# Performance work log

Hardware: AMD Instinct MI355X
Metric: run time of the kernel (lower is better)

Reference implementation:

```python
import jax, jax.numpy as jnp
import numpy as np

TAU = 100.0
DT = 1.0
NOISE_STD = 0.1
HID = 100


def setup_inputs() -> dict:
    key = jax.random.key(0)
    ks = jax.random.split(key, 7)
    T, B = 750, 1024
    input_seq = jax.random.normal(ks[0], (T, B, 4), dtype=jnp.float32)
    noise = jax.random.normal(ks[1], (T, B, HID), dtype=jnp.float32)
    # orthogonal recurrent weight J [H, H]
    a = jax.random.normal(ks[2], (HID, HID), dtype=jnp.float32)
    q, r = jnp.linalg.qr(a)
    J_w = q * jnp.sign(jnp.diag(r))[None, :]
    # input projection rows [b_m; b_c; b_cm; b_cc] -> [4, H] (xavier for (H,1) fan)
    bound_b = float(np.sqrt(6.0 / (HID + 1)))
    Bmat = jax.random.uniform(ks[3], (4, HID), jnp.float32, -bound_b, bound_b)
    c_x = jnp.zeros((HID,), dtype=jnp.float32)
    bound_w = float(np.sqrt(6.0 / (HID + 1)))
    Wout_w = jax.random.uniform(ks[4], (1, HID), jnp.float32, -bound_w, bound_w)
    Wout_b = jnp.zeros((1,), dtype=jnp.float32)
    return {"input_seq": input_seq, "noise": noise, "J_w": J_w,
            "Bmat": Bmat, "c_x": c_x, "Wout_w": Wout_w, "Wout_b": Wout_b}


def reference(input_seq, noise, J_w, Bmat, c_x, Wout_w, Wout_b):
    # input_seq: [T, B, 4], noise: [T, B, H]
    T, B, _ = input_seq.shape
    alpha = DT / TAU

    # precompute input drive for all steps: u_m@b_m^T + ... == u_t @ Bmat  [T, B, H]
    drive = jnp.einsum('tbi,ih->tbh', input_seq, Bmat)

    def step(x, inp):
        d_t, n_t = inp
        r = jnp.tanh(x)
        dx = alpha * (-x + r @ J_w.T + d_t + c_x + NOISE_STD * n_t)
        x = x + dx
        return x, None

    x0 = jnp.zeros((B, HID), dtype=input_seq.dtype)
    x_final, _ = jax.lax.scan(step, x0, (drive, noise))
    out = jnp.tanh(x_final) @ Wout_w.T + Wout_b  # [B, 1]
    return out.squeeze(-1)  # [B]
```

## Files before the change

kernel.cpp:

```cpp
#include <hip/hip_runtime.h>
#include <hip/hip_bf16.h>

#define HID 100
#define TT 750
#define NB_TOT 1024
#define ALPHA 0.01f
#define NSTD 0.1f

typedef __bf16 bf16x8 __attribute__((ext_vector_type(8)));
typedef float floatx4 __attribute__((ext_vector_type(4)));

__device__ __forceinline__ float fast_tanh(float v) {
    float e = __expf(2.0f * v);
    return 1.0f - 2.0f / (e + 1.0f);
}

__device__ __forceinline__ void wg_barrier() {
    asm volatile("s_waitcnt lgkmcnt(0)" ::: "memory");
    __builtin_amdgcn_s_barrier();
    asm volatile("" ::: "memory");
    __builtin_amdgcn_sched_barrier(0);
}

__global__ __launch_bounds__(256, 2)
void rnn_kernel(const float* __restrict__ useq,
                const float* __restrict__ noise,
                const float* __restrict__ Jw,
                const float* __restrict__ Bm,
                const float* __restrict__ cxp,
                const float* __restrict__ Ww,
                const float* __restrict__ Wb,
                float* __restrict__ out)
{
    __shared__ __align__(16) __bf16 rbuf[16 * 128];
    __shared__ float ybuf[2][112];
    __shared__ float red[256];

    const int tid  = threadIdx.x;
    const int wv   = tid >> 6;
    const int lane = tid & 63;
    const int wg   = blockIdx.x;

    const int  bb  = tid / 100;
    const int  hh  = tid % 100;
    const bool upd = (tid < 200);
    const int  gb  = wg * 2 + bb;

    float bm0=0.f, bm1=0.f, bm2=0.f, bm3=0.f, cx=0.f, wout=0.f;
    if (upd) {
        bm0 = Bm[0*HID + hh]; bm1 = Bm[1*HID + hh];
        bm2 = Bm[2*HID + hh]; bm3 = Bm[3*HID + hh];
        cx  = cxp[hh];
        wout = Ww[hh];
    }

    {
        floatx4 z = {0.f, 0.f, 0.f, 0.f};
        ((floatx4*)rbuf)[tid] = z;
    }

    const int m16 = lane & 15;
    const int q   = lane >> 4;
    bf16x8 jhi[2][4], jlo[2][4];
    #pragma unroll
    for (int ti = 0; ti < 2; ++ti) {
        const int tile = wv * 2 + ti;
        const int h = tile * 16 + m16;
        #pragma unroll
        for (int s = 0; s < 4; ++s) {
            bf16x8 vhi, vlo;
            #pragma unroll
            for (int j = 0; j < 8; ++j) {
                const int k = s * 32 + q * 8 + j;
                float v = (h < HID && k < HID) ? Jw[h * HID + k] : 0.0f;
                __bf16 hi = (__bf16)v;
                vhi[j] = hi;
                vlo[j] = (__bf16)(v - (float)hi);
            }
            jhi[ti][s] = vhi;
            jlo[ti][s] = vlo;
        }
    }

    const float* np = noise + (size_t)gb * HID + hh;
    const float* up = useq  + (size_t)gb * 4;
    float   nb0=0.f, nb1=0.f, nb2=0.f, nb3=0.f;
    floatx4 ub0={0,0,0,0}, ub1={0,0,0,0}, ub2={0,0,0,0}, ub3={0,0,0,0};
    if (upd) {
        nb0 = np[0 * (NB_TOT*HID)]; ub0 = *(const floatx4*)(up + 0 * (NB_TOT*4));
        nb1 = np[1 * (NB_TOT*HID)]; ub1 = *(const floatx4*)(up + 1 * (NB_TOT*4));
        nb2 = np[2 * (NB_TOT*HID)]; ub2 = *(const floatx4*)(up + 2 * (NB_TOT*4));
        nb3 = np[3 * (NB_TOT*HID)]; ub3 = *(const floatx4*)(up + 3 * (NB_TOT*4));
    }

    float x = 0.0f;
    __syncthreads();

    auto step = [&](int T, float& NB, floatx4& UB) {
        bf16x8 afr[4];
        const bf16x8* rb16 = (const bf16x8*)rbuf;
        #pragma unroll
        for (int s = 0; s < 4; ++s)
            afr[s] = rb16[m16 * 16 + ((s * 4 + q) ^ (lane & 7))];
        #pragma unroll
        for (int ti = 0; ti < 2; ++ti) {
            floatx4 acch = {0.f, 0.f, 0.f, 0.f};
            floatx4 accl = {0.f, 0.f, 0.f, 0.f};
            #pragma unroll
            for (int s = 0; s < 4; ++s) {
                acch = __builtin_amdgcn_mfma_f32_16x16x32_bf16(afr[s], jhi[ti][s], acch, 0, 0, 0);
                accl = __builtin_amdgcn_mfma_f32_16x16x32_bf16(afr[s], jlo[ti][s], accl, 0, 0, 0);
            }
            const int tile = wv * 2 + ti;
            if (tile < 7 && lane < 16) {
                ybuf[0][tile * 16 + lane] = acch[0] + accl[0];
                ybuf[1][tile * 16 + lane] = acch[1] + accl[1];
            }
        }
        wg_barrier();
        if (upd) {
            const float y = ybuf[bb][hh];
            const float d = UB[0]*bm0 + UB[1]*bm1 + UB[2]*bm2 + UB[3]*bm3;
            x = x * (1.0f - ALPHA) + ALPHA * (y + d + cx + NSTD * NB);
            const float r = fast_tanh(x);
            rbuf[bb * 128 + (((hh >> 3) ^ bb) << 3) + (hh & 7)] = (__bf16)r;
            const int tf = (T + 4 < TT) ? (T + 4) : (TT - 1);
            NB = np[tf * (NB_TOT*HID)];
            UB = *(const floatx4*)(up + tf * (NB_TOT*4));
        }
        wg_barrier();
    };

    for (int tb = 0; tb < 748; tb += 4) {
        step(tb + 0, nb0, ub0);
        step(tb + 1, nb1, ub1);
        step(tb + 2, nb2, ub2);
        step(tb + 3, nb3, ub3);
    }
    step(748, nb0, ub0);
    step(749, nb1, ub1);

    red[tid] = upd ? (fast_tanh(x) * wout) : 0.0f;
    __syncthreads();
    if (tid < 2) {
        float s2 = Wb[0];
        #pragma unroll 4
        for (int i = 0; i < HID; ++i) s2 += red[tid * HID + i];
        out[wg * 2 + tid] = s2;
    }
}

extern "C" void kernel_launch(void* const* d_in, const int* in_sizes, int n_in,
                              void* d_out, int out_size, void* d_ws, size_t ws_size,
                              hipStream_t stream) {
    rnn_kernel<<<dim3(512), dim3(256), 0, stream>>>(
        (const float*)d_in[0], (const float*)d_in[1], (const float*)d_in[2],
        (const float*)d_in[3], (const float*)d_in[4], (const float*)d_in[5],
        (const float*)d_in[6], (float*)d_out);
}
```

Measured before the change: 727.3 us.

## Update state in MFMA lanes and double-buffer r to use one barrier per step

```diff
diff --git a/kernel.cpp b/kernel.cpp
--- a/kernel.cpp
+++ b/kernel.cpp
@@ -21,6 +21,11 @@
     asm volatile("" ::: "memory");
     __builtin_amdgcn_sched_barrier(0);
 }
+
+struct Pf {
+    float n00, n01, n10, n11;
+    floatx4 u0, u1;
+};
 
 __global__ __launch_bounds__(256, 2)
 void rnn_kernel(const float* __restrict__ useq,
@@ -32,35 +37,44 @@
                 const float* __restrict__ Wb,
                 float* __restrict__ out)
 {
-    __shared__ __align__(16) __bf16 rbuf[16 * 128];
-    __shared__ float ybuf[2][112];
-    __shared__ float red[256];
+    __shared__ __align__(16) __bf16 rbuf[2][16 * 128];
+    __shared__ float red[2][112];
 
     const int tid  = threadIdx.x;
     const int wv   = tid >> 6;
     const int lane = tid & 63;
     const int wg   = blockIdx.x;
-
-    const int  bb  = tid / 100;
-    const int  hh  = tid % 100;
-    const bool upd = (tid < 200);
-    const int  gb  = wg * 2 + bb;
-
-    float bm0=0.f, bm1=0.f, bm2=0.f, bm3=0.f, cx=0.f, wout=0.f;
-    if (upd) {
-        bm0 = Bm[0*HID + hh]; bm1 = Bm[1*HID + hh];
-        bm2 = Bm[2*HID + hh]; bm3 = Bm[3*HID + hh];
-        cx  = cxp[hh];
-        wout = Ww[hh];
+    const int m16  = lane & 15;
+    const int q    = lane >> 4;
+
+    const int gb0 = wg * 2 + 0;
+    const int gb1 = wg * 2 + 1;
+
+    const int  hh0 = (wv * 2 + 0) * 16 + m16;
+    const int  hh1 = (wv * 2 + 1) * 16 + m16;
+    const bool act = (q == 0);
+    const bool v0  = act && (hh0 < HID);
+    const bool v1  = act && (hh1 < HID);
+    const int  h0c = (hh0 < HID) ? hh0 : 0;
+    const int  h1c = (hh1 < HID) ? hh1 : 0;
+
+    floatx4 bmA = {0,0,0,0}, bmB = {0,0,0,0};
+    float cx0 = 0.f, cx1 = 0.f, w0 = 0.f, w1 = 0.f;
+    if (v0) {
+        bmA = floatx4{Bm[0*HID+hh0], Bm[1*HID+hh0], Bm[2*HID+hh0], Bm[3*HID+hh0]};
+        cx0 = cxp[hh0]; w0 = Ww[hh0];
+    }
+    if (v1) {
+        bmB = floatx4{Bm[0*HID+hh1], Bm[1*HID+hh1], Bm[2*HID+hh1], Bm[3*HID+hh1]};
+        cx1 = cxp[hh1]; w1 = Ww[hh1];
     }
 
     {
         floatx4 z = {0.f, 0.f, 0.f, 0.f};
-        ((floatx4*)rbuf)[tid] = z;
-    }
-
-    const int m16 = lane & 15;
-    const int q   = lane >> 4;
+        ((floatx4*)rbuf)[tid]       = z;
+        ((floatx4*)rbuf)[tid + 256] = z;
+    }
+
     bf16x8 jhi[2][4], jlo[2][4];
     #pragma unroll
     for (int ti = 0; ti < 2; ++ti) {
@@ -82,70 +96,105 @@
         }
     }
 
-    const float* np = noise + (size_t)gb * HID + hh;
-    const float* up = useq  + (size_t)gb * 4;
-    float   nb0=0.f, nb1=0.f, nb2=0.f, nb3=0.f;
-    floatx4 ub0={0,0,0,0}, ub1={0,0,0,0}, ub2={0,0,0,0}, ub3={0,0,0,0};
-    if (upd) {
-        nb0 = np[0 * (NB_TOT*HID)]; ub0 = *(const floatx4*)(up + 0 * (NB_TOT*4));
-        nb1 = np[1 * (NB_TOT*HID)]; ub1 = *(const floatx4*)(up + 1 * (NB_TOT*4));
-        nb2 = np[2 * (NB_TOT*HID)]; ub2 = *(const floatx4*)(up + 2 * (NB_TOT*4));
-        nb3 = np[3 * (NB_TOT*HID)]; ub3 = *(const floatx4*)(up + 3 * (NB_TOT*4));
-    }
-
-    float x = 0.0f;
+    const int a00 = hh0;
+    const int a01 = 128 + (hh0 ^ 8);
+    const int a10 = hh1;
+    const int a11 = 128 + (hh1 ^ 8);
+
+    const float* np00 = noise + (size_t)gb0 * HID + h0c;
+    const float* np01 = noise + (size_t)gb1 * HID + h0c;
+    const float* np10 = noise + (size_t)gb0 * HID + h1c;
+    const float* np11 = noise + (size_t)gb1 * HID + h1c;
+    const float* up0  = useq  + (size_t)gb0 * 4;
+    const float* up1  = useq  + (size_t)gb1 * 4;
+
+    auto pfetch = [&](int t, Pf& P) {
+        if (act) {
+            const size_t tn = (size_t)t * (NB_TOT * HID);
+            const size_t tu = (size_t)t * (NB_TOT * 4);
+            P.n00 = np00[tn]; P.n01 = np01[tn];
+            P.n10 = np10[tn]; P.n11 = np11[tn];
+            P.u0 = *(const floatx4*)(up0 + tu);
+            P.u1 = *(const floatx4*)(up1 + tu);
+        }
+    };
+
+    Pf p0, p1, p2, p3;
+    pfetch(0, p0); pfetch(1, p1); pfetch(2, p2); pfetch(3, p3);
+
+    float x00 = 0.f, x01 = 0.f, x10 = 0.f, x11 = 0.f;
     __syncthreads();
 
-    auto step = [&](int T, float& NB, floatx4& UB) {
+    auto step = [&](int T, Pf& P, int pb) {
         bf16x8 afr[4];
-        const bf16x8* rb16 = (const bf16x8*)rbuf;
+        const bf16x8* rb16 = (const bf16x8*)(rbuf[pb]);
         #pragma unroll
         for (int s = 0; s < 4; ++s)
             afr[s] = rb16[m16 * 16 + ((s * 4 + q) ^ (lane & 7))];
-        #pragma unroll
-        for (int ti = 0; ti < 2; ++ti) {
-            floatx4 acch = {0.f, 0.f, 0.f, 0.f};
-            floatx4 accl = {0.f, 0.f, 0.f, 0.f};
+        float y00, y01, y10, y11;
+        {
+            floatx4 acch = {0,0,0,0}, accl = {0,0,0,0};
             #pragma unroll
             for (int s = 0; s < 4; ++s) {
-                acch = __builtin_amdgcn_mfma_f32_16x16x32_bf16(afr[s], jhi[ti][s], acch, 0, 0, 0);
-                accl = __builtin_amdgcn_mfma_f32_16x16x32_bf16(afr[s], jlo[ti][s], accl, 0, 0, 0);
-            }
-            const int tile = wv * 2 + ti;
-            if (tile < 7 && lane < 16) {
-                ybuf[0][tile * 16 + lane] = acch[0] + accl[0];
-                ybuf[1][tile * 16 + lane] = acch[1] + accl[1];
-            }
-        }
-        wg_barrier();
-        if (upd) {
-            const float y = ybuf[bb][hh];
-            const float d = UB[0]*bm0 + UB[1]*bm1 + UB[2]*bm2 + UB[3]*bm3;
-            x = x * (1.0f - ALPHA) + ALPHA * (y + d + cx + NSTD * NB);
-            const float r = fast_tanh(x);
-            rbuf[bb * 128 + (((hh >> 3) ^ bb) << 3) + (hh & 7)] = (__bf16)r;
+                acch = __builtin_amdgcn_mfma_f32_16x16x32_bf16(afr[s], jhi[0][s], acch, 0, 0, 0);
+                accl = __builtin_amdgcn_mfma_f32_16x16x32_bf16(afr[s], jlo[0][s], accl, 0, 0, 0);
+            }
+            y00 = acch[0] + accl[0]; y01 = acch[1] + accl[1];
+        }
+        {
+            floatx4 acch = {0,0,0,0}, accl = {0,0,0,0};
+            #pragma unroll
+            for (int s = 0; s < 4; ++s) {
+                acch = __builtin_amdgcn_mfma_f32_16x16x32_bf16(afr[s], jhi[1][s], acch, 0, 0, 0);
+                accl = __builtin_amdgcn_mfma_f32_16x16x32_bf16(afr[s], jlo[1][s], accl, 0, 0, 0);
+            }
+            y10 = acch[0] + accl[0]; y11 = acch[1] + accl[1];
+        }
+        __bf16* wb = rbuf[pb ^ 1];
+        if (act) {
+            if (v0) {
+                const float d0 = P.u0[0]*bmA[0] + P.u0[1]*bmA[1] + P.u0[2]*bmA[2] + P.u0[3]*bmA[3];
+                x00 = x00 * (1.0f - ALPHA) + ALPHA * (y00 + d0 + cx0 + NSTD * P.n00);
+                wb[a00] = (__bf16)fast_tanh(x00);
+                const float d1 = P.u1[0]*bmA[0] + P.u1[1]*bmA[1] + P.u1[2]*bmA[2] + P.u1[3]*bmA[3];
+                x01 = x01 * (1.0f - ALPHA) + ALPHA * (y01 + d1 + cx0 + NSTD * P.n01);
+                wb[a01] = (__bf16)fast_tanh(x01);
+            }
+            if (v1) {
+                const float d0 = P.u0[0]*bmB[0] + P.u0[1]*bmB[1] + P.u0[2]*bmB[2] + P.u0[3]*bmB[3];
+                x10 = x10 * (1.0f - ALPHA) + ALPHA * (y10 + d0 + cx1 + NSTD * P.n10);
+                wb[a10] = (__bf16)fast_tanh(x10);
+                const float d1 = P.u1[0]*bmB[0] + P.u1[1]*bmB[1] + P.u1[2]*bmB[2] + P.u1[3]*bmB[3];
+                x11 = x11 * (1.0f - ALPHA) + ALPHA * (y11 + d1 + cx1 + NSTD * P.n11);
+                wb[a11] = (__bf16)fast_tanh(x11);
+            }
             const int tf = (T + 4 < TT) ? (T + 4) : (TT - 1);
-            NB = np[tf * (NB_TOT*HID)];
-            UB = *(const floatx4*)(up + tf * (NB_TOT*4));
+            const size_t tn = (size_t)tf * (NB_TOT * HID);
+            const size_t tu = (size_t)tf * (NB_TOT * 4);
+            P.n00 = np00[tn]; P.n01 = np01[tn];
+            P.n10 = np10[tn]; P.n11 = np11[tn];
+            P.u0 = *(const floatx4*)(up0 + tu);
+            P.u1 = *(const floatx4*)(up1 + tu);
         }
         wg_barrier();
     };
 
     for (int tb = 0; tb < 748; tb += 4) {
-        step(tb + 0, nb0, ub0);
-        step(tb + 1, nb1, ub1);
-        step(tb + 2, nb2, ub2);
-        step(tb + 3, nb3, ub3);
-    }
-    step(748, nb0, ub0);
-    step(749, nb1, ub1);
-
-    red[tid] = upd ? (fast_tanh(x) * wout) : 0.0f;
+        step(tb + 0, p0, 0);
+        step(tb + 1, p1, 1);
+        step(tb + 2, p2, 0);
+        step(tb + 3, p3, 1);
+    }
+    step(748, p0, 0);
+    step(749, p1, 1);
+
+    if (v0) { red[0][hh0] = fast_tanh(x00) * w0; red[1][hh0] = fast_tanh(x01) * w0; }
+    if (v1) { red[0][hh1] = fast_tanh(x10) * w1; red[1][hh1] = fast_tanh(x11) * w1; }
     __syncthreads();
     if (tid < 2) {
         float s2 = Wb[0];
         #pragma unroll 4
-        for (int i = 0; i < HID; ++i) s2 += red[tid * HID + i];
+        for (int i = 0; i < HID; ++i) s2 += red[tid][i];
         out[wg * 2 + tid] = s2;
     }
 }
```

New measurement: 967.5 us. 1.33x slower.

## Use 32x32 MFMA with double-buffered state to halve per-step barriers

Applied to the files above, without the earlier changes.

```diff
diff --git a/kernel.cpp b/kernel.cpp
--- a/kernel.cpp
+++ b/kernel.cpp
@@ -9,6 +9,7 @@
 
 typedef __bf16 bf16x8 __attribute__((ext_vector_type(8)));
 typedef float floatx4 __attribute__((ext_vector_type(4)));
+typedef float floatx16 __attribute__((ext_vector_type(16)));
 
 __device__ __forceinline__ float fast_tanh(float v) {
     float e = __expf(2.0f * v);
@@ -22,6 +23,15 @@
     __builtin_amdgcn_sched_barrier(0);
 }
 
+__device__ __forceinline__ floatx16 zero16() {
+    floatx16 z;
+    #pragma unroll
+    for (int i = 0; i < 16; ++i) z[i] = 0.f;
+    return z;
+}
+
+struct Pf { float n0, n1; floatx4 u0, u1; };
+
 __global__ __launch_bounds__(256, 2)
 void rnn_kernel(const float* __restrict__ useq,
                 const float* __restrict__ noise,
@@ -32,121 +42,127 @@
                 const float* __restrict__ Wb,
                 float* __restrict__ out)
 {
-    __shared__ __align__(16) __bf16 rbuf[16 * 128];
-    __shared__ float ybuf[2][112];
-    __shared__ float red[256];
+    __shared__ __align__(16) __bf16 rbuf[2][2][128];
+    __shared__ float red[2][112];
 
     const int tid  = threadIdx.x;
     const int wv   = tid >> 6;
     const int lane = tid & 63;
+    const int l31  = lane & 31;
+    const int g    = lane >> 5;
     const int wg   = blockIdx.x;
+    const int gb0  = wg * 2;
 
-    const int  bb  = tid / 100;
-    const int  hh  = tid % 100;
-    const bool upd = (tid < 200);
-    const int  gb  = wg * 2 + bb;
+    const int  hh  = wv * 32 + l31;
+    const bool hv  = (hh < HID);
+    const bool act = (g == 0) && hv;
+    const int  hc  = hv ? hh : 0;
 
-    float bm0=0.f, bm1=0.f, bm2=0.f, bm3=0.f, cx=0.f, wout=0.f;
-    if (upd) {
-        bm0 = Bm[0*HID + hh]; bm1 = Bm[1*HID + hh];
-        bm2 = Bm[2*HID + hh]; bm3 = Bm[3*HID + hh];
-        cx  = cxp[hh];
-        wout = Ww[hh];
+    ((float*)rbuf)[tid] = 0.0f;
+
+    bf16x8 jhi[7], jlo[7];
+    #pragma unroll
+    for (int c = 0; c < 7; ++c) {
+        bf16x8 vh, vl;
+        #pragma unroll
+        for (int j = 0; j < 8; ++j) {
+            const int k = c * 16 + g * 8 + j;
+            float v = (hv && k < HID) ? Jw[hc * HID + k] : 0.0f;
+            __bf16 hi = (__bf16)v;
+            vh[j] = hi;
+            vl[j] = (__bf16)(v - (float)hi);
+        }
+        jhi[c] = vh; jlo[c] = vl;
     }
 
-    {
-        floatx4 z = {0.f, 0.f, 0.f, 0.f};
-        ((floatx4*)rbuf)[tid] = z;
+    floatx4 bm = {0,0,0,0};
+    float cx = 0.f, w = 0.f;
+    if (act) {
+        bm = floatx4{Bm[0*HID+hh], Bm[1*HID+hh], Bm[2*HID+hh], Bm[3*HID+hh]};
+        cx = cxp[hh]; w = Ww[hh];
     }
 
-    const int m16 = lane & 15;
-    const int q   = lane >> 4;
-    bf16x8 jhi[2][4], jlo[2][4];
-    #pragma unroll
-    for (int ti = 0; ti < 2; ++ti) {
-        const int tile = wv * 2 + ti;
-        const int h = tile * 16 + m16;
-        #pragma unroll
-        for (int s = 0; s < 4; ++s) {
-            bf16x8 vhi, vlo;
-            #pragma unroll
-            for (int j = 0; j < 8; ++j) {
-                const int k = s * 32 + q * 8 + j;
-                float v = (h < HID && k < HID) ? Jw[h * HID + k] : 0.0f;
-                __bf16 hi = (__bf16)v;
-                vhi[j] = hi;
-                vlo[j] = (__bf16)(v - (float)hi);
-            }
-            jhi[ti][s] = vhi;
-            jlo[ti][s] = vlo;
+    const float* npb = noise + (size_t)gb0 * HID + hc;
+    const float* upb = useq  + (size_t)gb0 * 4;
+
+    auto pfetch = [&](int t, Pf& P) {
+        if (act) {
+            const float* n = npb + (size_t)t * (NB_TOT * HID);
+            const float* u = upb + (size_t)t * (NB_TOT * 4);
+            P.n0 = n[0];  P.n1 = n[HID];
+            P.u0 = *(const floatx4*)u;
+            P.u1 = *(const floatx4*)(u + 4);
         }
-    }
+    };
 
-    const float* np = noise + (size_t)gb * HID + hh;
-    const float* up = useq  + (size_t)gb * 4;
-    float   nb0=0.f, nb1=0.f, nb2=0.f, nb3=0.f;
-    floatx4 ub0={0,0,0,0}, ub1={0,0,0,0}, ub2={0,0,0,0}, ub3={0,0,0,0};
-    if (upd) {
-        nb0 = np[0 * (NB_TOT*HID)]; ub0 = *(const floatx4*)(up + 0 * (NB_TOT*4));
-        nb1 = np[1 * (NB_TOT*HID)]; ub1 = *(const floatx4*)(up + 1 * (NB_TOT*4));
-        nb2 = np[2 * (NB_TOT*HID)]; ub2 = *(const floatx4*)(up + 2 * (NB_TOT*4));
-        nb3 = np[3 * (NB_TOT*HID)]; ub3 = *(const floatx4*)(up + 3 * (NB_TOT*4));
-    }
+    Pf p0, p1, p2, p3;
+    pfetch(0, p0); pfetch(1, p1); pfetch(2, p2); pfetch(3, p3);
 
-    float x = 0.0f;
+    float x0 = 0.f, x1 = 0.f;
     __syncthreads();
 
-    auto step = [&](int T, float& NB, floatx4& UB) {
-        bf16x8 afr[4];
-        const bf16x8* rb16 = (const bf16x8*)rbuf;
+    const int aidx = (lane & 1) * 16 + g;
+
+    auto stepf = [&](int T, Pf& P, int pb) {
+        const bf16x8* rb = (const bf16x8*)(rbuf[pb]);
+        bf16x8 afr[7];
         #pragma unroll
-        for (int s = 0; s < 4; ++s)
-            afr[s] = rb16[m16 * 16 + ((s * 4 + q) ^ (lane & 7))];
-        #pragma unroll
-        for (int ti = 0; ti < 2; ++ti) {
-            floatx4 acch = {0.f, 0.f, 0.f, 0.f};
-            floatx4 accl = {0.f, 0.f, 0.f, 0.f};
-            #pragma unroll
-            for (int s = 0; s < 4; ++s) {
-                acch = __builtin_amdgcn_mfma_f32_16x16x32_bf16(afr[s], jhi[ti][s], acch, 0, 0, 0);
-                accl = __builtin_amdgcn_mfma_f32_16x16x32_bf16(afr[s], jlo[ti][s], accl, 0, 0, 0);
-            }
-            const int tile = wv * 2 + ti;
-            if (tile < 7 && lane < 16) {
-                ybuf[0][tile * 16 + lane] = acch[0] + accl[0];
-                ybuf[1][tile * 16 + lane] = acch[1] + accl[1];
-            }
+        for (int c = 0; c < 7; ++c) afr[c] = rb[aidx + c * 2];
+        float base0 = 0.f, base1 = 0.f;
+        if (act) {
+            const float d0 = P.u0[0]*bm[0] + P.u0[1]*bm[1] + P.u0[2]*bm[2] + P.u0[3]*bm[3];
+            const float d1 = P.u1[0]*bm[0] + P.u1[1]*bm[1] + P.u1[2]*bm[2] + P.u1[3]*bm[3];
+            base0 = x0 * (1.0f - ALPHA) + ALPHA * (d0 + cx + NSTD * P.n0);
+            base1 = x1 * (1.0f - ALPHA) + ALPHA * (d1 + cx + NSTD * P.n1);
         }
-        wg_barrier();
-        if (upd) {
-            const float y = ybuf[bb][hh];
-            const float d = UB[0]*bm0 + UB[1]*bm1 + UB[2]*bm2 + UB[3]*bm3;
-            x = x * (1.0f - ALPHA) + ALPHA * (y + d + cx + NSTD * NB);
-            const float r = fast_tanh(x);
-            rbuf[bb * 128 + (((hh >> 3) ^ bb) << 3) + (hh & 7)] = (__bf16)r;
-            const int tf = (T + 4 < TT) ? (T + 4) : (TT - 1);
-            NB = np[tf * (NB_TOT*HID)];
-            UB = *(const floatx4*)(up + tf * (NB_TOT*4));
+        floatx16 hA = zero16(), hB = zero16(), lA = zero16(), lB = zero16();
+        hA = __builtin_amdgcn_mfma_f32_32x32x16_bf16(afr[0], jhi[0], hA, 0, 0, 0);
+        lA = __builtin_amdgcn_mfma_f32_32x32x16_bf16(afr[0], jlo[0], lA, 0, 0, 0);
+        hB = __builtin_amdgcn_mfma_f32_32x32x16_bf16(afr[4], jhi[4], hB, 0, 0, 0);
+        lB = __builtin_amdgcn_mfma_f32_32x32x16_bf16(afr[4], jlo[4], lB, 0, 0, 0);
+        hA = __builtin_amdgcn_mfma_f32_32x32x16_bf16(afr[1], jhi[1], hA, 0, 0, 0);
+        lA = __builtin_amdgcn_mfma_f32_32x32x16_bf16(afr[1], jlo[1], lA, 0, 0, 0);
+        hB = __builtin_amdgcn_mfma_f32_32x32x16_bf16(afr[5], jhi[5], hB, 0, 0, 0);
+        lB = __builtin_amdgcn_mfma_f32_32x32x16_bf16(afr[5], jlo[5], lB, 0, 0, 0);
+        hA = __builtin_amdgcn_mfma_f32_32x32x16_bf16(afr[2], jhi[2], hA, 0, 0, 0);
+        lA = __builtin_amdgcn_mfma_f32_32x32x16_bf16(afr[2], jlo[2], lA, 0, 0, 0);
+        hB = __builtin_amdgcn_mfma_f32_32x32x16_bf16(afr[6], jhi[6], hB, 0, 0, 0);
+        lB = __builtin_amdgcn_mfma_f32_32x32x16_bf16(afr[6], jlo[6], lB, 0, 0, 0);
+        hA = __builtin_amdgcn_mfma_f32_32x32x16_bf16(afr[3], jhi[3], hA, 0, 0, 0);
+        lA = __builtin_amdgcn_mfma_f32_32x32x16_bf16(afr[3], jlo[3], lA, 0, 0, 0);
+        if (act) {
+            const float y0 = (hA[0] + hB[0]) + (lA[0] + lB[0]);
+            const float y1 = (hA[1] + hB[1]) + (lA[1] + lB[1]);
+            x0 = base0 + ALPHA * y0;
+            x1 = base1 + ALPHA * y1;
+            __bf16* wb = (__bf16*)(rbuf[pb ^ 1]);
+            wb[hh]       = (__bf16)fast_tanh(x0);
+            wb[128 + hh] = (__bf16)fast_tanh(x1);
         }
+        const int tf = T + 4;
+        if (tf < TT) pfetch(tf, P);
         wg_barrier();
     };
 
     for (int tb = 0; tb < 748; tb += 4) {
-        step(tb + 0, nb0, ub0);
-        step(tb + 1, nb1, ub1);
-        step(tb + 2, nb2, ub2);
-        step(tb + 3, nb3, ub3);
+        stepf(tb + 0, p0, 0);
+        stepf(tb + 1, p1, 1);
+        stepf(tb + 2, p2, 0);
+        stepf(tb + 3, p3, 1);
     }
-    step(748, nb0, ub0);
-    step(749, nb1, ub1);
+    stepf(748, p0, 0);
+    stepf(749, p1, 1);
 
-    red[tid] = upd ? (fast_tanh(x) * wout) : 0.0f;
+    if (act) {
+        red[0][hh] = fast_tanh(x0) * w;
+        red[1][hh] = fast_tanh(x1) * w;
+    }
     __syncthreads();
     if (tid < 2) {
         float s2 = Wb[0];
         #pragma unroll 4
-        for (int i = 0; i < HID; ++i) s2 += red[tid * HID + i];
-        out[wg * 2 + tid] = s2;
+        for (int i = 0; i < HID; ++i) s2 += red[tid][i];
+        out[gb0 + tid] = s2;
     }
 }
 
```

Measured after the change: 1.051 ms. 1.45x slower.

## Process four batch rows per workgroup using unused MFMA rows

Applied to the files above, without the earlier changes.

```diff
diff --git a/kernel.cpp b/kernel.cpp
--- a/kernel.cpp
+++ b/kernel.cpp
@@ -22,7 +22,9 @@
     __builtin_amdgcn_sched_barrier(0);
 }
 
-__global__ __launch_bounds__(256, 2)
+struct Pf { float n0, n2; floatx4 u0, u2; };
+
+__global__ __launch_bounds__(256, 1)
 void rnn_kernel(const float* __restrict__ useq,
                 const float* __restrict__ noise,
                 const float* __restrict__ Jw,
@@ -33,8 +35,8 @@
                 float* __restrict__ out)
 {
     __shared__ __align__(16) __bf16 rbuf[16 * 128];
-    __shared__ float ybuf[2][112];
-    __shared__ float red[256];
+    __shared__ float ybuf[4][112];
+    __shared__ float red[4][112];
 
     const int tid  = threadIdx.x;
     const int wv   = tid >> 6;
@@ -44,7 +46,7 @@
     const int  bb  = tid / 100;
     const int  hh  = tid % 100;
     const bool upd = (tid < 200);
-    const int  gb  = wg * 2 + bb;
+    const int  gb  = wg * 4 + bb;
 
     float bm0=0.f, bm1=0.f, bm2=0.f, bm3=0.f, cx=0.f, wout=0.f;
     if (upd) {
@@ -84,19 +86,25 @@
 
     const float* np = noise + (size_t)gb * HID + hh;
     const float* up = useq  + (size_t)gb * 4;
-    float   nb0=0.f, nb1=0.f, nb2=0.f, nb3=0.f;
-    floatx4 ub0={0,0,0,0}, ub1={0,0,0,0}, ub2={0,0,0,0}, ub3={0,0,0,0};
-    if (upd) {
-        nb0 = np[0 * (NB_TOT*HID)]; ub0 = *(const floatx4*)(up + 0 * (NB_TOT*4));
-        nb1 = np[1 * (NB_TOT*HID)]; ub1 = *(const floatx4*)(up + 1 * (NB_TOT*4));
-        nb2 = np[2 * (NB_TOT*HID)]; ub2 = *(const floatx4*)(up + 2 * (NB_TOT*4));
-        nb3 = np[3 * (NB_TOT*HID)]; ub3 = *(const floatx4*)(up + 3 * (NB_TOT*4));
-    }
 
-    float x = 0.0f;
+    auto pfetch = [&](int t, Pf& P) {
+        if (upd) {
+            const float* n = np + (size_t)t * (NB_TOT * HID);
+            const float* u = up + (size_t)t * (NB_TOT * 4);
+            P.n0 = n[0];
+            P.n2 = n[2 * HID];
+            P.u0 = *(const floatx4*)u;
+            P.u2 = *(const floatx4*)(u + 8);
+        }
+    };
+
+    Pf p0, p1, p2, p3;
+    pfetch(0, p0); pfetch(1, p1); pfetch(2, p2); pfetch(3, p3);
+
+    float x0 = 0.0f, x2 = 0.0f;
     __syncthreads();
 
-    auto step = [&](int T, float& NB, floatx4& UB) {
+    auto step = [&](int T, Pf& P) {
         bf16x8 afr[4];
         const bf16x8* rb16 = (const bf16x8*)rbuf;
         #pragma unroll
@@ -115,45 +123,53 @@
             if (tile < 7 && lane < 16) {
                 ybuf[0][tile * 16 + lane] = acch[0] + accl[0];
                 ybuf[1][tile * 16 + lane] = acch[1] + accl[1];
+                ybuf[2][tile * 16 + lane] = acch[2] + accl[2];
+                ybuf[3][tile * 16 + lane] = acch[3] + accl[3];
             }
         }
         wg_barrier();
         if (upd) {
-            const float y = ybuf[bb][hh];
-            const float d = UB[0]*bm0 + UB[1]*bm1 + UB[2]*bm2 + UB[3]*bm3;
-            x = x * (1.0f - ALPHA) + ALPHA * (y + d + cx + NSTD * NB);
-            const float r = fast_tanh(x);
-            rbuf[bb * 128 + (((hh >> 3) ^ bb) << 3) + (hh & 7)] = (__bf16)r;
+            const float y0 = ybuf[bb][hh];
+            const float y2 = ybuf[bb + 2][hh];
+            const float d0 = P.u0[0]*bm0 + P.u0[1]*bm1 + P.u0[2]*bm2 + P.u0[3]*bm3;
+            const float d2 = P.u2[0]*bm0 + P.u2[1]*bm1 + P.u2[2]*bm2 + P.u2[3]*bm3;
+            x0 = x0 * (1.0f - ALPHA) + ALPHA * (y0 + d0 + cx + NSTD * P.n0);
+            x2 = x2 * (1.0f - ALPHA) + ALPHA * (y2 + d2 + cx + NSTD * P.n2);
+            const int c = hh >> 3, e = hh & 7;
+            rbuf[ bb      * 128 + ((c ^  bb     ) << 3) + e] = (__bf16)fast_tanh(x0);
+            rbuf[(bb + 2) * 128 + ((c ^ (bb + 2)) << 3) + e] = (__bf16)fast_tanh(x2);
             const int tf = (T + 4 < TT) ? (T + 4) : (TT - 1);
-            NB = np[tf * (NB_TOT*HID)];
-            UB = *(const floatx4*)(up + tf * (NB_TOT*4));
+            pfetch(tf, P);
         }
         wg_barrier();
     };
 
     for (int tb = 0; tb < 748; tb += 4) {
-        step(tb + 0, nb0, ub0);
-        step(tb + 1, nb1, ub1);
-        step(tb + 2, nb2, ub2);
-        step(tb + 3, nb3, ub3);
+        step(tb + 0, p0);
+        step(tb + 1, p1);
+        step(tb + 2, p2);
+        step(tb + 3, p3);
     }
-    step(748, nb0, ub0);
-    step(749, nb1, ub1);
+    step(748, p0);
+    step(749, p1);
 
-    red[tid] = upd ? (fast_tanh(x) * wout) : 0.0f;
+    if (upd) {
+        red[bb][hh]     = fast_tanh(x0) * wout;
+        red[bb + 2][hh] = fast_tanh(x2) * wout;
+    }
     __syncthreads();
-    if (tid < 2) {
+    if (tid < 4) {
         float s2 = Wb[0];
         #pragma unroll 4
-        for (int i = 0; i < HID; ++i) s2 += red[tid * HID + i];
-        out[wg * 2 + tid] = s2;
+        for (int i = 0; i < HID; ++i) s2 += red[tid][i];
+        out[wg * 4 + tid] = s2;
     }
 }
 
 extern "C" void kernel_launch(void* const* d_in, const int* in_sizes, int n_in,
                               void* d_out, int out_size, void* d_ws, size_t ws_size,
                               hipStream_t stream) {
-    rnn_kernel<<<dim3(512), dim3(256), 0, stream>>>(
+    rnn_kernel<<<dim3(256), dim3(256), 0, stream>>>(
         (const float*)d_in[0], (const float*)d_in[1], (const float*)d_in[2],
         (const float*)d_in[3], (const float*)d_in[4], (const float*)d_in[5],
         (const float*)d_in[6], (float*)d_out);
```

Result: slower. 763.6 us (+5.0%).
